# Performance work log

Measured on AMD Instinct MI355X. Metric: run time of the kernel, lower is better.

## Reference

```python
import jax, jax.numpy as jnp
import numpy as np

MIN_MZ, MAX_MZ, BIN_W = 0.0, 1000.0, 0.01
NUM_BINS = int((MAX_MZ - MIN_MZ) / BIN_W)      # 100000
GROUP, OUT_PER_GROUP = 30, 3
GROUPS = NUM_BINS // GROUP                      # 3333
BINNER_OUT = GROUPS * OUT_PER_GROUP             # 9999
SCALING = 0.5
EPS = 1e-6
B, P = 256, 512                                 # pairs, padded peaks per spectrum


def setup_inputs() -> dict:
    key = jax.random.key(0)
    ks = jax.random.split(key, 10)
    # mz drawn in [0, 1100): peaks >= max_mz are dropped by the range filter (ragged-like)
    mz = jax.random.uniform(ks[0], (B, 2, P), jnp.float32, 0.0, 1100.0)
    intensities = jax.random.uniform(ks[1], (B, 2, P), jnp.float32, 1e-3, 1.0)
    s = 0.02
    return dict(
        mz=mz,
        intensities=intensities,
        binner_w=jax.random.normal(ks[2], (GROUPS, GROUP, OUT_PER_GROUP), jnp.float32) * s,
        binner_b=jax.random.normal(ks[3], (GROUPS, OUT_PER_GROUP), jnp.float32) * s,
        w0=jax.random.normal(ks[4], (BINNER_OUT, 1000), jnp.float32) * s,
        b0=jnp.zeros((1000,), jnp.float32),
        w1=jax.random.normal(ks[5], (1000, 800), jnp.float32) * s,
        b1=jnp.zeros((800,), jnp.float32),
        w2=jax.random.normal(ks[6], (800, 800), jnp.float32) * s,
        b2=jnp.zeros((800,), jnp.float32),
        we=jax.random.normal(ks[7], (800, 400), jnp.float32) * s,
        be=jnp.zeros((400,), jnp.float32),
    )


def _bin_spectra(mz, inten):
    # mz, inten: [N, P] -> binned [N, NUM_BINS] via ragged scatter-add of inten**SCALING
    mzc = jax.lax.stop_gradient(mz)             # indices are non-differentiable
    mask = (mzc >= MIN_MZ) & (mzc < MAX_MZ)
    idx = jnp.clip(((mzc - MIN_MZ) / BIN_W).astype(jnp.int32), 0, NUM_BINS - 1)
    vals = jnp.where(mask, inten ** SCALING, 0.0)
    n = mz.shape[0]
    rows = jnp.arange(n)[:, None]               # [N,1] broadcast against [N,P]
    binned = jnp.zeros((n, NUM_BINS), jnp.float32)
    return binned.at[rows, idx].add(vals)


def _encoder(binned, binner_w, binner_b, w0, b0, w1, b1, w2, b2, we, be):
    n = binned.shape[0]
    # PeakBinner: block-diagonal micro-linears over groups of 30 bins (last 10 bins unused)
    xg = binned[:, : GROUPS * GROUP].reshape(n, GROUPS, GROUP)
    x = jnp.einsum('bgi,gio->bgo', xg, binner_w) + binner_b
    x = x.reshape(n, BINNER_OUT)
    x = jax.nn.relu(x @ w0 + b0)
    x = jax.nn.relu(x @ w1 + b1)                # dropout = identity at eval
    x = jax.nn.relu(x @ w2 + b2)
    return x @ we + be                           # [N, 400]


def reference(mz, intensities, binner_w, binner_b, w0, b0, w1, b1, w2, b2, we, be):
    bp = mz.shape[0]
    n = bp * 2
    binned = _bin_spectra(mz.reshape(n, P), intensities.reshape(n, P))
    emb = _encoder(binned, binner_w, binner_b, w0, b0, w1, b1, w2, b2, we, be)
    emb = emb.reshape(bp, 2, -1)
    e1, e2 = emb[:, 0], emb[:, 1]
    n1 = jnp.maximum(jnp.linalg.norm(e1, axis=1), EPS)
    n2 = jnp.maximum(jnp.linalg.norm(e2, axis=1), EPS)
    return jnp.sum(e1 * e2, axis=1) / (n1 * n2)  # [B] cosine similarity
```

## Files before the change

### kernel.cpp

```cpp
#include <hip/hip_runtime.h>

typedef __bf16 bf16;
typedef __bf16 bf16x8 __attribute__((ext_vector_type(8)));
typedef float  f32x4  __attribute__((ext_vector_type(4)));

#define NSPEC   512
#define BOUT    9999
#define K0A     10240
#define N00     1024
#define KSPLIT0 16

__device__ __forceinline__ void gload_lds16(const bf16* g, bf16* l) {
    auto* gp = reinterpret_cast<const __attribute__((address_space(1))) unsigned int*>(
        reinterpret_cast<uintptr_t>(g));
    auto* lp = reinterpret_cast<__attribute__((address_space(3))) unsigned int*>(
        reinterpret_cast<uintptr_t>(l));
    __builtin_amdgcn_global_load_lds(gp, lp, 16, 0, 0);
}

__device__ __forceinline__ void transpose_tile64(const float* __restrict__ src,
                                                 bf16* __restrict__ dst,
                                                 int K, int N, int K0,
                                                 float* tile, int bx, int by) {
    int n0 = bx * 64, k0 = by * 32;
    int t = threadIdx.x;
    {
        int kr = t >> 4, nc = (t & 15) * 4;
        int gk = k0 + kr, gn = n0 + nc;
        float4 v;
        if (gk < K && gn + 3 < N) {
            v = *reinterpret_cast<const float4*>(src + (size_t)gk * N + gn);
        } else {
            v.x = (gk < K && gn + 0 < N) ? src[(size_t)gk * N + gn + 0] : 0.f;
            v.y = (gk < K && gn + 1 < N) ? src[(size_t)gk * N + gn + 1] : 0.f;
            v.z = (gk < K && gn + 2 < N) ? src[(size_t)gk * N + gn + 2] : 0.f;
            v.w = (gk < K && gn + 3 < N) ? src[(size_t)gk * N + gn + 3] : 0.f;
        }
        tile[kr * 65 + nc + 0] = v.x;
        tile[kr * 65 + nc + 1] = v.y;
        tile[kr * 65 + nc + 2] = v.z;
        tile[kr * 65 + nc + 3] = v.w;
    }
    __syncthreads();
    {
        int nr = t >> 3, kc = (t & 7) * 4;
        bf16 v[4];
#pragma unroll
        for (int e = 0; e < 4; ++e) v[e] = (bf16)tile[(kc + e) * 65 + nr];
        *(ushort4*)&dst[(size_t)(n0 + nr) * K0 + k0 + kc] = *(ushort4*)v;
    }
}

__global__ __launch_bounds__(512) void prep_all(const float* __restrict__ mz,
                                                const float* __restrict__ inten,
                                                const float* __restrict__ bw,
                                                const float* __restrict__ bb,
                                                const float* __restrict__ w0,
                                                const float* __restrict__ w1,
                                                const float* __restrict__ w2,
                                                const float* __restrict__ we,
                                                bf16* __restrict__ A,
                                                bf16* __restrict__ B0t,
                                                bf16* __restrict__ B1t,
                                                bf16* __restrict__ B2t,
                                                bf16* __restrict__ BEt,
                                                bf16* __restrict__ H1b,
                                                bf16* __restrict__ H2b,
                                                float* __restrict__ psums) {
    __shared__ float smem[K0A];
    int b = blockIdx.x;
    if (b < 5120) {
        transpose_tile64(w0, B0t, BOUT, 1000, K0A, smem, b & 15, b >> 4);
    } else if (b < 5568) {
        int r = b - 5120;
        transpose_tile64(w1, B1t, 1000, 800, 1024, smem, r % 14, r / 14);
    } else if (b < 6016) {
        int r = b - 5568;
        transpose_tile64(w2, B2t, 800, 800, 1024, smem, r % 14, r / 14);
    } else if (b < 6240) {
        int r = b - 6016;
        transpose_tile64(we, BEt, 800, 400, 1024, smem, r % 7, r / 7);
    } else if (b < 6752) {
        const int spec = b - 6240;
        const int t = threadIdx.x;
#pragma unroll
        for (int i = 0; i < 5; ++i)
            *(float4*)&smem[(i * 512 + t) * 4] = float4{0.f, 0.f, 0.f, 0.f};
        __syncthreads();
        {
            float m = mz[(size_t)spec * 512 + t];
            float v = inten[(size_t)spec * 512 + t];
            bool mask = (m >= 0.0f) && (m < 1000.0f);
            int idx = (int)(m / 0.01f);
            idx = min(max(idx, 0), 99999);
            if (mask && idx < 99990) {
                int g = idx / 30;
                float val = sqrtf(v);
                const float* w = bw + (size_t)idx * 3;
                atomicAdd(&smem[g * 3 + 0], val * w[0]);
                atomicAdd(&smem[g * 3 + 1], val * w[1]);
                atomicAdd(&smem[g * 3 + 2], val * w[2]);
            }
        }
        __syncthreads();
        bf16* Arow = A + (size_t)spec * K0A;
#pragma unroll
        for (int i = 0; i < 5; ++i) {
            int c = (i * 512 + t) * 4;
            float4 s = *(const float4*)&smem[c];
            bf16 o[4];
            o[0] = (bf16)((c + 0 < BOUT) ? bb[c + 0] + s.x : 0.f);
            o[1] = (bf16)((c + 1 < BOUT) ? bb[c + 1] + s.y : 0.f);
            o[2] = (bf16)((c + 2 < BOUT) ? bb[c + 2] + s.z : 0.f);
            o[3] = (bf16)((c + 3 < BOUT) ? bb[c + 3] + s.w : 0.f);
            *(ushort4*)&Arow[c] = *(ushort4*)o;
        }
    } else if (b < 6784) {
        int idx = b - 6752;
        bf16* H = (idx < 16) ? H1b : H2b;
        int sub = idx & 15;
        int t = threadIdx.x;
        int row = sub * 32 + (t >> 4);
        int col = 896 + (t & 15) * 8;
        *(uint4*)&H[(size_t)row * 1024 + col] = uint4{0u, 0u, 0u, 0u};
    } else {
        for (int i = threadIdx.x; i < 1024; i += 512) psums[i] = 0.f;
    }
}

__global__ __launch_bounds__(512) void gemm0_splitk(const bf16* __restrict__ A,
                                                    const bf16* __restrict__ Bt,
                                                    bf16* __restrict__ Cslab) {
    constexpr int K0 = K0A, KITERS = 10, BK = 64;
    __shared__ __align__(16) bf16 As[2][128 * BK];
    __shared__ __align__(16) bf16 Bs[2][128 * BK];
    const int bid = blockIdx.x;
    const int kp = bid & 15;
    const int tile = bid >> 4;
    const int mt = tile & 3, nt = tile >> 2;
    const int tid = threadIdx.x, wave = tid >> 6, lane = tid & 63;
    const int wm = wave & 1, wn = wave >> 1;
    const int lrow = lane & 15, quad = lane >> 4;

    const bf16* Ag = A  + (size_t)(mt * 128) * K0 + kp * (KITERS * BK);
    const bf16* Bg = Bt + (size_t)(nt * 128) * K0 + kp * (KITERS * BK);

    auto stage = [&](int buf, int kk) {
        const int k = kk * BK;
        const int lr = lane >> 3;
        const int lch = lane & 7;
#pragma unroll
        for (int j = 0; j < 2; ++j) {
            int row0 = j * 64 + wave * 8;
            int row = row0 + lr;
            int ch  = lch ^ (row & 7);
            gload_lds16(Ag + (size_t)row * K0 + k + ch * 8, &As[buf][row0 * BK]);
        }
#pragma unroll
        for (int j = 0; j < 2; ++j) {
            int row0 = j * 64 + wave * 8;
            int row = row0 + lr;
            int ch  = lch ^ (row & 7);
            gload_lds16(Bg + (size_t)row * K0 + k + ch * 8, &Bs[buf][row0 * BK]);
        }
    };

    f32x4 acc[4][2] = {};
    stage(0, 0);
    for (int kk = 0; kk < KITERS; ++kk) {
        const int cur = kk & 1;
        __syncthreads();
        if (kk + 1 < KITERS) stage(cur ^ 1, kk + 1);
#pragma unroll
        for (int ks = 0; ks < 2; ++ks) {
            bf16x8 af[4], bfr[2];
            const int c = ks * 4 + quad;
#pragma unroll
            for (int im = 0; im < 4; ++im) {
                int r = wm * 64 + im * 16 + lrow;
                af[im] = *(const bf16x8*)&As[cur][r * BK + ((c ^ (r & 7)) << 3)];
            }
#pragma unroll
            for (int in = 0; in < 2; ++in) {
                int r = wn * 32 + in * 16 + lrow;
                bfr[in] = *(const bf16x8*)&Bs[cur][r * BK + ((c ^ (r & 7)) << 3)];
            }
#pragma unroll
            for (int im = 0; im < 4; ++im)
#pragma unroll
                for (int in = 0; in < 2; ++in)
                    acc[im][in] = __builtin_amdgcn_mfma_f32_16x16x32_bf16(af[im], bfr[in], acc[im][in], 0, 0, 0);
        }
    }
    bf16* C = Cslab + (size_t)kp * (NSPEC * N00);
#pragma unroll
    for (int im = 0; im < 4; ++im) {
        int row0 = mt * 128 + wm * 64 + im * 16 + quad * 4;
#pragma unroll
        for (int in = 0; in < 2; ++in) {
            int col = nt * 128 + wn * 32 + in * 16 + lrow;
#pragma unroll
            for (int r = 0; r < 4; ++r)
                C[(size_t)(row0 + r) * N00 + col] = (bf16)acc[im][in][r];
        }
    }
}

__global__ __launch_bounds__(256) void reduce_bias_relu(const bf16* __restrict__ Cslab,
                                                        const float* __restrict__ b0,
                                                        bf16* __restrict__ H0b) {
    int idx = blockIdx.x * 256 + threadIdx.x;
    int r = idx >> 7, c = (idx & 127) * 8;
    float s[8] = {};
#pragma unroll
    for (int kp = 0; kp < KSPLIT0; ++kp) {
        bf16x8 v = *(const bf16x8*)&Cslab[(size_t)kp * (NSPEC * N00) + (size_t)r * N00 + c];
#pragma unroll
        for (int j = 0; j < 8; ++j) s[j] += (float)v[j];
    }
    bf16 o[8];
#pragma unroll
    for (int j = 0; j < 8; ++j)
        o[j] = (bf16)fmaxf(s[j] + ((c + j < 1000) ? b0[c + j] : 0.f), 0.f);
    *(uint4*)&H0b[(size_t)r * N00 + c] = *(uint4*)o;
}

template <bool LAST>
__global__ __launch_bounds__(512) void gemm_tail(const bf16* __restrict__ A,
                                                 const bf16* __restrict__ Bt,
                                                 const float* __restrict__ bias,
                                                 bf16* __restrict__ Ob,
                                                 float* __restrict__ psums,
                                                 unsigned* __restrict__ done,
                                                 float* __restrict__ out,
                                                 int Nreal, int ntiles) {
    constexpr int BK = 256, KITERS = 4;
    __shared__ __align__(16) bf16 As[2][32 * BK];
    __shared__ __align__(16) bf16 Bs[2][32 * BK];
    __shared__ f32x4 xacc[4][64];
    __shared__ unsigned lastf;
    const int bid = blockIdx.x;
    const int mt = bid / ntiles, nt = bid % ntiles;
    const int tid = threadIdx.x, wave = tid >> 6, lane = tid & 63;
    const int g = wave >> 2, w2 = wave & 3;
    const int wm = w2 & 1, wn = w2 >> 1;
    const int lrow = lane & 15, quad = lane >> 4;

    const bf16* Ag = A  + (size_t)(mt * 32) * 1024;
    const bf16* Bg = Bt + (size_t)(nt * 32) * 1024;

    auto stage = [&](int buf, int kk) {
        const int k = kk * BK;
#pragma unroll
        for (int j = 0; j < 2; ++j) {
            int row0 = (wave + j * 8) * 2;
            int row = row0 + (lane >> 5);
            int ch  = (lane & 31) ^ (row & 31);
            gload_lds16(Ag + (size_t)row * 1024 + k + ch * 8, &As[buf][row0 * BK]);
            gload_lds16(Bg + (size_t)row * 1024 + k + ch * 8, &Bs[buf][row0 * BK]);
        }
    };

    f32x4 acc = {};
    stage(0, 0);
    for (int kk = 0; kk < KITERS; ++kk) {
        const int cur = kk & 1;
        __syncthreads();
        if (kk + 1 < KITERS) stage(cur ^ 1, kk + 1);
#pragma unroll
        for (int ks = 0; ks < 4; ++ks) {
            int ra = wm * 16 + lrow, rb = wn * 16 + lrow;
            int c = g * 16 + ks * 4 + quad;
            bf16x8 af  = *(const bf16x8*)&As[cur][ra * BK + ((c ^ (ra & 31)) << 3)];
            bf16x8 bfr = *(const bf16x8*)&Bs[cur][rb * BK + ((c ^ (rb & 31)) << 3)];
            acc = __builtin_amdgcn_mfma_f32_16x16x32_bf16(af, bfr, acc, 0, 0, 0);
        }
    }
    __syncthreads();
    if (g == 1) xacc[w2][lane] = acc;
    __syncthreads();
    if (g == 0) {
        f32x4 o = xacc[w2][lane];
        acc[0] += o[0]; acc[1] += o[1]; acc[2] += o[2]; acc[3] += o[3];
        int row0 = mt * 32 + wm * 16 + quad * 4;
        int col  = nt * 32 + wn * 16 + lrow;
        if (!LAST) {
            float bv = (col < Nreal) ? bias[col] : 0.f;
#pragma unroll
            for (int r = 0; r < 4; ++r)
                Ob[(size_t)(row0 + r) * 1024 + col] = (bf16)fmaxf(acc[r] + bv, 0.f);
        } else {
            bool valid = (col < 400);
            float bv = valid ? bias[col] : 0.f;
            float v[4];
#pragma unroll
            for (int r = 0; r < 4; ++r) v[r] = valid ? (acc[r] + bv) : 0.f;
            int p0 = row0 >> 1;
            float sums[6] = {v[0] * v[1], v[0] * v[0], v[1] * v[1],
                             v[2] * v[3], v[2] * v[2], v[3] * v[3]};
#pragma unroll
            for (int off = 1; off < 16; off <<= 1)
#pragma unroll
                for (int s = 0; s < 6; ++s) sums[s] += __shfl_xor(sums[s], off);
            if (lrow == 0) {
#pragma unroll
                for (int s = 0; s < 3; ++s) {
                    atomicAdd(&psums[(p0 + 0) * 3 + s], sums[s]);
                    atomicAdd(&psums[(p0 + 1) * 3 + s], sums[3 + s]);
                }
            }
        }
    }
    if (LAST) {
        __syncthreads();
        if (tid == 0) {
            __threadfence();
            unsigned old = __hip_atomic_fetch_add(done, 1u, __ATOMIC_ACQ_REL,
                                                  __HIP_MEMORY_SCOPE_AGENT);
            lastf = (old == 223u) ? 1u : 0u;
        }
        __syncthreads();
        if (lastf && tid < 256) {
            float d  = __hip_atomic_load(&psums[tid * 3 + 0], __ATOMIC_RELAXED, __HIP_MEMORY_SCOPE_AGENT);
            float s1 = __hip_atomic_load(&psums[tid * 3 + 1], __ATOMIC_RELAXED, __HIP_MEMORY_SCOPE_AGENT);
            float s2 = __hip_atomic_load(&psums[tid * 3 + 2], __ATOMIC_RELAXED, __HIP_MEMORY_SCOPE_AGENT);
            float n1 = fmaxf(sqrtf(s1), 1e-6f);
            float n2 = fmaxf(sqrtf(s2), 1e-6f);
            out[tid] = d / (n1 * n2);
        }
    }
}

extern "C" void kernel_launch(void* const* d_in, const int* in_sizes, int n_in,
                              void* d_out, int out_size, void* d_ws, size_t ws_size,
                              hipStream_t stream) {
    const float* mz    = (const float*)d_in[0];
    const float* inten = (const float*)d_in[1];
    const float* bw    = (const float*)d_in[2];
    const float* bb    = (const float*)d_in[3];
    const float* w0    = (const float*)d_in[4];
    const float* b0    = (const float*)d_in[5];
    const float* w1    = (const float*)d_in[6];
    const float* b1    = (const float*)d_in[7];
    const float* w2    = (const float*)d_in[8];
    const float* b2    = (const float*)d_in[9];
    const float* we    = (const float*)d_in[10];
    const float* be    = (const float*)d_in[11];
    float* out = (float*)d_out;

    char* ws = (char*)d_ws;
    size_t off = 0;
    auto alloc = [&](size_t bytes) { char* p = ws + off; off += (bytes + 255) & ~(size_t)255; return p; };
    bf16*  A     = (bf16*) alloc((size_t)NSPEC * K0A * 2);
    bf16*  B0t   = (bf16*) alloc((size_t)N00 * K0A * 2);
    bf16*  B1t   = (bf16*) alloc((size_t)896 * 1024 * 2);
    bf16*  B2t   = (bf16*) alloc((size_t)896 * 1024 * 2);
    bf16*  BEt   = (bf16*) alloc((size_t)448 * 1024 * 2);
    bf16*  Cslab = (bf16*) alloc((size_t)KSPLIT0 * NSPEC * N00 * 2);
    bf16*  H0b   = (bf16*) alloc((size_t)NSPEC * 1024 * 2);
    bf16*  H1b   = (bf16*) alloc((size_t)NSPEC * 1024 * 2);
    bf16*  H2b   = (bf16*) alloc((size_t)NSPEC * 1024 * 2);
    float* psums = (float*)alloc(1024 * 4);
    unsigned* done = (unsigned*)(psums + 768);

    prep_all<<<6785, 512, 0, stream>>>(mz, inten, bw, bb, w0, w1, w2, we,
                                       A, B0t, B1t, B2t, BEt, H1b, H2b, psums);
    gemm0_splitk<<<512, 512, 0, stream>>>(A, B0t, Cslab);
    reduce_bias_relu<<<256, 256, 0, stream>>>(Cslab, b0, H0b);
    gemm_tail<false><<<448, 512, 0, stream>>>(H0b, B1t, b1, H1b, nullptr, nullptr, nullptr, 800, 28);
    gemm_tail<false><<<448, 512, 0, stream>>>(H1b, B2t, b2, H2b, nullptr, nullptr, nullptr, 800, 28);
    gemm_tail<true ><<<224, 512, 0, stream>>>(H2b, BEt, be, nullptr, psums, done, out, 400, 14);
}
```

Before: 163.3 us.

## Double transpose tile depth and widen tail GEMM tiles to 32x64 without intra-block split-K

Measured after the change: 163.0 us (median of 2 runs). No clear change (-0.2%).

```diff
diff --git a/kernel.cpp b/kernel.cpp
--- a/kernel.cpp
+++ b/kernel.cpp
@@ -22,32 +22,36 @@
                                                  bf16* __restrict__ dst,
                                                  int K, int N, int K0,
                                                  float* tile, int bx, int by) {
-    int n0 = bx * 64, k0 = by * 32;
+    int n0 = bx * 64, k0 = by * 64;
     int t = threadIdx.x;
     {
-        int kr = t >> 4, nc = (t & 15) * 4;
-        int gk = k0 + kr, gn = n0 + nc;
-        float4 v;
-        if (gk < K && gn + 3 < N) {
-            v = *reinterpret_cast<const float4*>(src + (size_t)gk * N + gn);
-        } else {
-            v.x = (gk < K && gn + 0 < N) ? src[(size_t)gk * N + gn + 0] : 0.f;
-            v.y = (gk < K && gn + 1 < N) ? src[(size_t)gk * N + gn + 1] : 0.f;
-            v.z = (gk < K && gn + 2 < N) ? src[(size_t)gk * N + gn + 2] : 0.f;
-            v.w = (gk < K && gn + 3 < N) ? src[(size_t)gk * N + gn + 3] : 0.f;
-        }
-        tile[kr * 65 + nc + 0] = v.x;
-        tile[kr * 65 + nc + 1] = v.y;
-        tile[kr * 65 + nc + 2] = v.z;
-        tile[kr * 65 + nc + 3] = v.w;
+        int kr = t >> 3, fc = (t & 7) * 8;
+        int gk = k0 + kr;
+#pragma unroll
+        for (int h = 0; h < 2; ++h) {
+            int gn = n0 + fc + h * 4;
+            float4 v;
+            if (gk < K && gn + 3 < N) {
+                v = *reinterpret_cast<const float4*>(src + (size_t)gk * N + gn);
+            } else {
+                v.x = (gk < K && gn + 0 < N) ? src[(size_t)gk * N + gn + 0] : 0.f;
+                v.y = (gk < K && gn + 1 < N) ? src[(size_t)gk * N + gn + 1] : 0.f;
+                v.z = (gk < K && gn + 2 < N) ? src[(size_t)gk * N + gn + 2] : 0.f;
+                v.w = (gk < K && gn + 3 < N) ? src[(size_t)gk * N + gn + 3] : 0.f;
+            }
+            tile[kr * 65 + fc + h * 4 + 0] = v.x;
+            tile[kr * 65 + fc + h * 4 + 1] = v.y;
+            tile[kr * 65 + fc + h * 4 + 2] = v.z;
+            tile[kr * 65 + fc + h * 4 + 3] = v.w;
+        }
     }
     __syncthreads();
     {
-        int nr = t >> 3, kc = (t & 7) * 4;
-        bf16 v[4];
-#pragma unroll
-        for (int e = 0; e < 4; ++e) v[e] = (bf16)tile[(kc + e) * 65 + nr];
-        *(ushort4*)&dst[(size_t)(n0 + nr) * K0 + k0 + kc] = *(ushort4*)v;
+        int nr = t >> 3, kc = (t & 7) * 8;
+        bf16 v[8];
+#pragma unroll
+        for (int e = 0; e < 8; ++e) v[e] = (bf16)tile[(kc + e) * 65 + nr];
+        *(uint4*)&dst[(size_t)(n0 + nr) * K0 + k0 + kc] = *(uint4*)v;
     }
 }
 
@@ -69,19 +73,19 @@
                                                 float* __restrict__ psums) {
     __shared__ float smem[K0A];
     int b = blockIdx.x;
-    if (b < 5120) {
+    if (b < 2560) {
         transpose_tile64(w0, B0t, BOUT, 1000, K0A, smem, b & 15, b >> 4);
-    } else if (b < 5568) {
-        int r = b - 5120;
+    } else if (b < 2784) {
+        int r = b - 2560;
         transpose_tile64(w1, B1t, 1000, 800, 1024, smem, r % 14, r / 14);
-    } else if (b < 6016) {
-        int r = b - 5568;
+    } else if (b < 3008) {
+        int r = b - 2784;
         transpose_tile64(w2, B2t, 800, 800, 1024, smem, r % 14, r / 14);
-    } else if (b < 6240) {
-        int r = b - 6016;
+    } else if (b < 3120) {
+        int r = b - 3008;
         transpose_tile64(we, BEt, 800, 400, 1024, smem, r % 7, r / 7);
-    } else if (b < 6752) {
-        const int spec = b - 6240;
+    } else if (b < 3632) {
+        const int spec = b - 3120;
         const int t = threadIdx.x;
 #pragma unroll
         for (int i = 0; i < 5; ++i)
@@ -115,8 +119,8 @@
             o[3] = (bf16)((c + 3 < BOUT) ? bb[c + 3] + s.w : 0.f);
             *(ushort4*)&Arow[c] = *(ushort4*)o;
         }
-    } else if (b < 6784) {
-        int idx = b - 6752;
+    } else if (b < 3664) {
+        int idx = b - 3632;
         bf16* H = (idx < 16) ? H1b : H2b;
         int sub = idx & 15;
         int t = threadIdx.x;
@@ -236,18 +240,16 @@
                                                  int Nreal, int ntiles) {
     constexpr int BK = 256, KITERS = 4;
     __shared__ __align__(16) bf16 As[2][32 * BK];
-    __shared__ __align__(16) bf16 Bs[2][32 * BK];
-    __shared__ f32x4 xacc[4][64];
+    __shared__ __align__(16) bf16 Bs[2][64 * BK];
     __shared__ unsigned lastf;
     const int bid = blockIdx.x;
     const int mt = bid / ntiles, nt = bid % ntiles;
     const int tid = threadIdx.x, wave = tid >> 6, lane = tid & 63;
-    const int g = wave >> 2, w2 = wave & 3;
-    const int wm = w2 & 1, wn = w2 >> 1;
+    const int wm = wave & 1, wn = wave >> 1;
     const int lrow = lane & 15, quad = lane >> 4;
 
     const bf16* Ag = A  + (size_t)(mt * 32) * 1024;
-    const bf16* Bg = Bt + (size_t)(nt * 32) * 1024;
+    const bf16* Bg = Bt + (size_t)(nt * 64) * 1024;
 
     auto stage = [&](int buf, int kk) {
         const int k = kk * BK;
@@ -257,6 +259,12 @@
             int row = row0 + (lane >> 5);
             int ch  = (lane & 31) ^ (row & 31);
             gload_lds16(Ag + (size_t)row * 1024 + k + ch * 8, &As[buf][row0 * BK]);
+        }
+#pragma unroll
+        for (int j = 0; j < 4; ++j) {
+            int row0 = (wave + j * 8) * 2;
+            int row = row0 + (lane >> 5);
+            int ch  = (lane & 31) ^ (row & 31);
             gload_lds16(Bg + (size_t)row * 1024 + k + ch * 8, &Bs[buf][row0 * BK]);
         }
     };
@@ -268,22 +276,17 @@
         __syncthreads();
         if (kk + 1 < KITERS) stage(cur ^ 1, kk + 1);
 #pragma unroll
-        for (int ks = 0; ks < 4; ++ks) {
+        for (int ks = 0; ks < 8; ++ks) {
             int ra = wm * 16 + lrow, rb = wn * 16 + lrow;
-            int c = g * 16 + ks * 4 + quad;
+            int c = ks * 4 + quad;
             bf16x8 af  = *(const bf16x8*)&As[cur][ra * BK + ((c ^ (ra & 31)) << 3)];
             bf16x8 bfr = *(const bf16x8*)&Bs[cur][rb * BK + ((c ^ (rb & 31)) << 3)];
             acc = __builtin_amdgcn_mfma_f32_16x16x32_bf16(af, bfr, acc, 0, 0, 0);
         }
     }
-    __syncthreads();
-    if (g == 1) xacc[w2][lane] = acc;
-    __syncthreads();
-    if (g == 0) {
-        f32x4 o = xacc[w2][lane];
-        acc[0] += o[0]; acc[1] += o[1]; acc[2] += o[2]; acc[3] += o[3];
+    {
         int row0 = mt * 32 + wm * 16 + quad * 4;
-        int col  = nt * 32 + wn * 16 + lrow;
+        int col  = nt * 64 + wn * 16 + lrow;
         if (!LAST) {
             float bv = (col < Nreal) ? bias[col] : 0.f;
 #pragma unroll
@@ -317,7 +320,7 @@
             __threadfence();
             unsigned old = __hip_atomic_fetch_add(done, 1u, __ATOMIC_ACQ_REL,
                                                   __HIP_MEMORY_SCOPE_AGENT);
-            lastf = (old == 223u) ? 1u : 0u;
+            lastf = (old == 111u) ? 1u : 0u;
         }
         __syncthreads();
         if (lastf && tid < 256) {
@@ -363,11 +366,11 @@
     float* psums = (float*)alloc(1024 * 4);
     unsigned* done = (unsigned*)(psums + 768);
 
-    prep_all<<<6785, 512, 0, stream>>>(mz, inten, bw, bb, w0, w1, w2, we,
+    prep_all<<<3665, 512, 0, stream>>>(mz, inten, bw, bb, w0, w1, w2, we,
                                        A, B0t, B1t, B2t, BEt, H1b, H2b, psums);
     gemm0_splitk<<<512, 512, 0, stream>>>(A, B0t, Cslab);
     reduce_bias_relu<<<256, 256, 0, stream>>>(Cslab, b0, H0b);
-    gemm_tail<false><<<448, 512, 0, stream>>>(H0b, B1t, b1, H1b, nullptr, nullptr, nullptr, 800, 28);
-    gemm_tail<false><<<448, 512, 0, stream>>>(H1b, B2t, b2, H2b, nullptr, nullptr, nullptr, 800, 28);
-    gemm_tail<true ><<<224, 512, 0, stream>>>(H2b, BEt, be, nullptr, psums, done, out, 400, 14);
-}
+    gemm_tail<false><<<224, 512, 0, stream>>>(H0b, B1t, b1, H1b, nullptr, nullptr, nullptr, 800, 14);
+    gemm_tail<false><<<224, 512, 0, stream>>>(H1b, B2t, b2, H2b, nullptr, nullptr, nullptr, 800, 14);
+    gemm_tail<true ><<<112, 512, 0, stream>>>(H2b, BEt, be, nullptr, psums, done, out, 400, 7);
+}
```
